# Kernel optimization log

Hardware: AMD Instinct MI355X
Metric: run time of the kernel (lower is better)

## Reference

```python
import jax, jax.numpy as jnp
import numpy as np

C_IN = 256
C_OUT = 256
NUM_HEADS = 4
C_HEAD = C_OUT // NUM_HEADS  # 64
ALPHA = 0.2
NEG_FILL = -9e15


def setup_inputs() -> dict:
    key = jax.random.key(0)
    k1, k2, k3, k4, k5 = jax.random.split(key, 5)
    B, N = 1, 4096
    node_feats = jax.random.normal(k1, (B, N, C_IN), dtype=jnp.float32)
    adj_matrix = jax.random.randint(k2, (B, N, N), 0, 2, dtype=jnp.int32)
    # xavier_uniform with gain=1.414 on projection weight (fan_in=C_IN, fan_out=C_OUT)
    lim_w = 1.414 * np.sqrt(6.0 / (C_IN + C_OUT))
    W = jax.random.uniform(k3, (C_IN, C_OUT), dtype=jnp.float32, minval=-lim_w, maxval=lim_w)
    b = jnp.zeros((C_OUT,), dtype=jnp.float32)
    lim_a = 1.414 * np.sqrt(6.0 / (NUM_HEADS + 2 * C_HEAD))
    a = jax.random.uniform(k4, (NUM_HEADS, 2 * C_HEAD), dtype=jnp.float32, minval=-lim_a, maxval=lim_a)
    return {"node_feats": node_feats, "adj_matrix": adj_matrix, "W": W, "b": b, "a": a}


def reference(node_feats, adj_matrix, W, b, a):
    B, N, _ = node_feats.shape
    # linear projection -> (B, N, H, C_HEAD)
    feats = (node_feats @ W + b).reshape(B, N, NUM_HEADS, C_HEAD)
    # attention logit for edge (i -> j): a_src . h_i + a_dst . h_j, per head
    a_src, a_dst = a[:, :C_HEAD], a[:, C_HEAD:]
    src = jnp.einsum('bnhc,hc->bnh', feats, a_src)  # indexed by row i
    dst = jnp.einsum('bnhc,hc->bnh', feats, a_dst)  # indexed by col j
    logits = src[:, :, None, :] + dst[:, None, :, :]  # (B, N, N, H)
    logits = jnp.where(logits >= 0, logits, ALPHA * logits)  # LeakyReLU(0.2)
    attn = jnp.where(adj_matrix[..., None] == 1, logits, NEG_FILL)
    probs = jax.nn.softmax(attn, axis=2)  # softmax over source nodes j
    out = jnp.einsum('bijh,bjhc->bihc', probs, feats)
    return out.reshape(B, N, NUM_HEADS * C_HEAD)  # concat heads
```

## Files before the change

### kernel.cpp

```cpp
#include <hip/hip_runtime.h>

#define NN 4096
#define C 256
#define NH 4
#define CH 64
#define JSPLIT 8
#define JSLICE (NN / JSPLIT)
#define NJT (JSLICE / 32)

typedef float f32x4 __attribute__((ext_vector_type(4)));
typedef __bf16 b16x8 __attribute__((ext_vector_type(8)));
typedef unsigned short u16x8 __attribute__((ext_vector_type(8)));
typedef unsigned int u32x4 __attribute__((ext_vector_type(4)));
typedef int i32x4 __attribute__((ext_vector_type(4)));
typedef _Float16 f16x2 __attribute__((ext_vector_type(2)));

#if __has_builtin(__builtin_amdgcn_raw_buffer_load_v4f32)
#define FBUF 1
#else
#define FBUF 0
#endif

__device__ inline float fast_exp2(float x) {
#if __has_builtin(__builtin_amdgcn_exp2f)
  return __builtin_amdgcn_exp2f(x);
#else
  return exp2f(x);
#endif
}

__device__ inline unsigned pack2bf(float f0, float f1) {
  unsigned u0 = __float_as_uint(f0) + 0x8000u;
  unsigned u1 = __float_as_uint(f1) + 0x8000u;
  return __builtin_amdgcn_perm(u1, u0, 0x07060302u);
}

__device__ inline unsigned cvtpk(float f0, float f1) {
  unsigned r;
  asm("v_cvt_pk_bf16_f32 %0, %1, %2" : "=v"(r) : "v"(f0), "v"(f1));
  return r;
}

__global__ __launch_bounds__(256) void k_prep(
    const float* __restrict__ X, const float* __restrict__ W,
    unsigned short* __restrict__ Xbf, unsigned short* __restrict__ WT) {
  const int b = blockIdx.x, t = threadIdx.x;
  if (b < 1024) {
    const int idx = b * 256 + t;
    const float4 v = ((const float4*)X)[idx];
    uint2 st;
    st.x = pack2bf(v.x, v.y);
    st.y = pack2bf(v.z, v.w);
    ((uint2*)Xbf)[idx] = st;
  } else {
    const int c = b - 1024;
    const float w = W[(size_t)t * C + c];
    WT[(size_t)c * C + t] = (unsigned short)((__float_as_uint(w) + 0x8000u) >> 16);
  }
}

__global__ __launch_bounds__(256) void k_feats(
    const unsigned short* __restrict__ Xbf, const unsigned short* __restrict__ WT,
    const float* __restrict__ bias, const float* __restrict__ av,
    const int* __restrict__ adj, unsigned char* __restrict__ packed,
    unsigned short* __restrict__ F, float2* __restrict__ srcAB,
    float* __restrict__ Ed) {
  if (blockIdx.x >= 256) {
    const int idx = (blockIdx.x - 256) * 256 + threadIdx.x;
    const int4 a0 = *(const int4*)(adj + (size_t)idx * 8);
    const int4 a1 = *(const int4*)(adj + (size_t)idx * 8 + 4);
    unsigned m = 0;
    m |= (a0.x != 0) ? 1u : 0u;   m |= (a0.y != 0) ? 2u : 0u;
    m |= (a0.z != 0) ? 4u : 0u;   m |= (a0.w != 0) ? 8u : 0u;
    m |= (a1.x != 0) ? 16u : 0u;  m |= (a1.y != 0) ? 32u : 0u;
    m |= (a1.z != 0) ? 64u : 0u;  m |= (a1.w != 0) ? 128u : 0u;
    const int newidx = (idx & ~63) | ((idx & 3) << 4) | ((idx >> 2) & 15);
    packed[newidx] = (unsigned char)m;
    return;
  }
  const int i0 = blockIdx.x * 16;
  const int h = threadIdx.x >> 6;
  const int lane = threadIdx.x & 63;
  const int q = lane >> 4, n = lane & 15;
  const int c0 = h * CH;
  const float LOG2E = 1.4426950408889634f;

  const f32x4 zero = {0.f, 0.f, 0.f, 0.f};
  f32x4 acc[4];
#pragma unroll
  for (int g = 0; g < 4; ++g) acc[g] = zero;

  const unsigned short* ap = Xbf + (size_t)(i0 + n) * C + q * 8;
#pragma unroll
  for (int kt = 0; kt < 8; ++kt) {
    const b16x8 aF = __builtin_bit_cast(b16x8, *(const u16x8*)(ap + kt * 32));
#pragma unroll
    for (int g = 0; g < 4; ++g) {
      const b16x8 bF = __builtin_bit_cast(b16x8,
          *(const u16x8*)(WT + (size_t)(c0 + g * 16 + n) * C + kt * 32 + q * 8));
      acc[g] = __builtin_amdgcn_mfma_f32_16x16x32_bf16(aF, bF, acc[g], 0, 0, 0);
    }
  }

  float fb[4][4], asv[4], adv[4];
#pragma unroll
  for (int g = 0; g < 4; ++g) {
    const float bs = bias[c0 + g * 16 + n];
    asv[g] = av[h * 128 + g * 16 + n];
    adv[g] = av[h * 128 + 64 + g * 16 + n];
#pragma unroll
    for (int r = 0; r < 4; ++r) fb[g][r] = acc[g][r] + bs;
  }
  const int jt = i0 >> 5, half = (i0 >> 4) & 1;
  const int qp = half * 2 + (q >> 1);
#pragma unroll
  for (int g = 0; g < 4; ++g) {
    uint2 st;
    st.x = pack2bf(fb[g][0], fb[g][1]);
    st.y = pack2bf(fb[g][2], fb[g][3]);
    *(uint2*)(F + ((size_t)((jt * NH + h) * 4 + g)) * 512 + (qp * 16 + n) * 8 + 4 * (q & 1)) = st;
  }
#pragma unroll
  for (int r = 0; r < 4; ++r) {
    float p = 0.f, d = 0.f;
#pragma unroll
    for (int g = 0; g < 4; ++g) {
      p = fmaf(fb[g][r], asv[g], p);
      d = fmaf(fb[g][r], adv[g], d);
    }
#pragma unroll
    for (int m = 1; m < 16; m <<= 1) {
      p += __shfl_xor(p, m);
      d += __shfl_xor(d, m);
    }
    if (n == 0) {
      const int row = i0 + q * 4 + r;
      const float dL = d * LOG2E;
      Ed[(size_t)h * NN + row] = fast_exp2(dL);
      Ed[(size_t)NH * NN + (size_t)h * NN + row] = fast_exp2(0.2f * dL);
      const float x = p + 16.0f;
      const float m2 = fmaxf(x, 0.2f * x) * LOG2E;
      srcAB[(size_t)row * NH + h] = make_float2(
          fast_exp2(fmaf(p, LOG2E, -m2)),
          fast_exp2(fmaf(0.2f * p, LOG2E, -m2)));
    }
  }
}

__global__ __launch_bounds__(256, 4) void k_attn(
    const unsigned char* __restrict__ packed,
    const unsigned short* __restrict__ F,
    const float2* __restrict__ srcAB, const float* __restrict__ Ed,
    _Float16* __restrict__ pacc, float* __restrict__ lpart) {
  __shared__ float sEd[NH * 2 * JSLICE];

  const int slice = blockIdx.x;
  const int i0 = blockIdx.y * 16;
  const int tid = threadIdx.x;
  const int h = tid >> 6;
  const int lane = tid & 63;
  const int q = lane >> 4, n = lane & 15;
  const int jbase = slice * JSLICE;

#pragma unroll
  for (int v = 0; v < 4; ++v) {
    const int idx = v * 256 + lane * 4;
    const int pl = idx >> 9, j = idx & 511;
    const float4 vv = *(const float4*)(Ed + (size_t)pl * NH * NN
                                       + (size_t)h * NN + jbase + j);
    *(float4*)(&sEd[h * 1024 + idx]) = vv;
  }

  const int r0 = i0 + n;
  const float2 ab0 = srcAB[(size_t)r0 * NH + h];

  const f32x4 zero = {0.f, 0.f, 0.f, 0.f};
  f32x4 acc[4], lacc = zero;
#pragma unroll
  for (int g = 0; g < 4; ++g) acc[g] = zero;

  u16x8 ou;
#pragma unroll
  for (int jj = 0; jj < 8; ++jj) ou[jj] = 0x3F80;
  const b16x8 ones = __builtin_bit_cast(b16x8, ou);

  const u32x4 m4 = *(const u32x4*)(packed + (size_t)r0 * 512 + (jbase >> 3) + q * 16);

#if FBUF
  i32x4 frsrc;
  frsrc[0] = (int)(unsigned)(size_t)F;
  frsrc[1] = (int)(((size_t)F >> 32) & 0xFFFFu);
  frsrc[2] = (int)0xFFFFFFFFu;
  frsrc[3] = 0x00020000;
  const unsigned fvoff =
      ((unsigned)((jbase >> 5) * 16 + h * 4)) * 1024u + (unsigned)lane * 16u;
#else
  const unsigned short* fp = F + ((size_t)((jbase >> 5) * NH + h) * 4) * 512 + lane * 8;
#endif
  const float* sB = &sEd[h * 1024];

  __syncthreads();

#pragma unroll
  for (int jt = 0; jt < NJT; ++jt) {
    const unsigned Mb = (m4[jt >> 2] >> ((jt & 3) * 8)) & 0xffu;

    const int off = jt * 32 + q * 8;
    const f32x4 eA[2] = { *(const f32x4*)(sB + off), *(const f32x4*)(sB + off + 4) };
    const f32x4 eB[2] = { *(const f32x4*)(sB + 512 + off),
                          *(const f32x4*)(sB + 512 + off + 4) };

    u32x4 pk;
#pragma unroll
    for (int hf = 0; hf < 2; ++hf) {
      const f32x4 xa = eA[hf] * ab0.x;
      const f32x4 xb = eB[hf] * ab0.y;
      float e[4];
#pragma unroll
      for (int t2 = 0; t2 < 4; ++t2) {
        const unsigned bit = 1u << (hf * 4 + t2);
        e[t2] = (Mb & bit) ? fmaxf(xa[t2], xb[t2]) : 0.f;
      }
      pk[hf * 2]     = cvtpk(e[0], e[1]);
      pk[hf * 2 + 1] = cvtpk(e[2], e[3]);
    }
    const b16x8 E = __builtin_bit_cast(b16x8, pk);
#pragma unroll
    for (int g = 0; g < 4; ++g) {
#if FBUF
      const f32x4 bv = __builtin_amdgcn_raw_buffer_load_v4f32(
          frsrc, fvoff + (unsigned)jt * 16384u + (unsigned)g * 1024u, 0, 0);
      const b16x8 bF = __builtin_bit_cast(b16x8, bv);
#else
      const b16x8 bF = __builtin_bit_cast(b16x8,
          *(const u16x8*)(fp + (size_t)(jt * NH * 4 + g) * 512));
#endif
      acc[g] = __builtin_amdgcn_mfma_f32_16x16x32_bf16(E, bF, acc[g], 0, 0, 0);
    }
    lacc = __builtin_amdgcn_mfma_f32_16x16x32_bf16(E, ones, lacc, 0, 0, 0);
  }

#pragma unroll
  for (int g = 0; g < 4; ++g)
#pragma unroll
    for (int r = 0; r < 4; ++r) {
      const int col = h * CH + g * 16 + n;
      pacc[((size_t)slice * NN + i0 + q * 4 + r) * C + col] = (_Float16)acc[g][r];
    }
  if (n == 0) {
#pragma unroll
    for (int r = 0; r < 4; ++r)
      lpart[((size_t)slice * NN + i0 + q * 4 + r) * NH + h] = lacc[r];
  }
}

__global__ __launch_bounds__(256) void k_final(
    const _Float16* __restrict__ pacc, const float* __restrict__ lpart,
    float* __restrict__ out) {
  const int t = threadIdx.x;
  const int row = blockIdx.x * 2 + (t >> 7);
  const int tc = t & 127;
  const int c2 = tc * 2;
  const int h = tc >> 5;
  float l = 0.f, sa0 = 0.f, sa1 = 0.f;
#pragma unroll
  for (int sp = 0; sp < JSPLIT; ++sp) {
    l += lpart[((size_t)sp * NN + row) * NH + h];
    const f16x2 v = *(const f16x2*)(pacc + ((size_t)sp * NN + row) * C + c2);
    sa0 += (float)v[0];
    sa1 += (float)v[1];
  }
  const float rl = 1.0f / l;
  *(float2*)(out + (size_t)row * C + c2) = make_float2(sa0 * rl, sa1 * rl);
}

extern "C" void kernel_launch(void* const* d_in, const int* in_sizes, int n_in,
                              void* d_out, int out_size, void* d_ws, size_t ws_size,
                              hipStream_t stream) {
  const float* nf   = (const float*)d_in[0];
  const int* adj    = (const int*)d_in[1];
  const float* W    = (const float*)d_in[2];
  const float* bias = (const float*)d_in[3];
  const float* av   = (const float*)d_in[4];
  float* out = (float*)d_out;

  char* ws = (char*)d_ws;
  unsigned char* packed  = (unsigned char*)ws;
  unsigned short* Xbf    = (unsigned short*)(ws + (2u << 20));
  unsigned short* WT     = (unsigned short*)(ws + (4u << 20));
  unsigned short* F      = (unsigned short*)(ws + (4u << 20) + (256u << 10));
  float2* srcAB = (float2*)(ws + (6u << 20) + (256u << 10));
  float* Ed     = (float*)(ws + (6u << 20) + (384u << 10));
  float* lpart  = (float*)(ws + (6u << 20) + (512u << 10));
  _Float16* pacc = (_Float16*)(ws + (8u << 20));

  k_prep<<<1280, 256, 0, stream>>>(nf, W, Xbf, WT);
  k_feats<<<8448, 256, 0, stream>>>(Xbf, WT, bias, av, adj, packed, F, srcAB, Ed);
  dim3 g2(JSPLIT, NN / 16);
  k_attn<<<g2, 256, 0, stream>>>(packed, F, srcAB, Ed, pacc, lpart);
  k_final<<<NN / 2, 256, 0, stream>>>(pacc, lpart, out);
}
```

Measured before the change: 137.1 us.

## Process two 16-row tiles per attention block to reuse feature loads

Each k_attn block now handles 32 destination rows instead of 16. Every loaded B-fragment of projected features and every shared-memory Ed read feeds two MFMA chains, and the grid shrinks by half. This halves global feature traffic and the per-block Ed staging per output row, at the cost of more accumulator registers, which may lower occupancy under launch_bounds(256,4), and fewer blocks in the grid.

Measured after the change: 135.4 us. Within noise of the previous version (-1.3%).

```diff
diff --git a/kernel.cpp b/kernel.cpp
--- a/kernel.cpp
+++ b/kernel.cpp
@@ -155,7 +155,7 @@
   __shared__ float sEd[NH * 2 * JSLICE];
 
   const int slice = blockIdx.x;
-  const int i0 = blockIdx.y * 16;
+  const int i0 = blockIdx.y * 32;
   const int tid = threadIdx.x;
   const int h = tid >> 6;
   const int lane = tid & 63;
@@ -171,20 +171,22 @@
     *(float4*)(&sEd[h * 1024 + idx]) = vv;
   }
 
-  const int r0 = i0 + n;
+  const int r0 = i0 + n, r1 = i0 + 16 + n;
   const float2 ab0 = srcAB[(size_t)r0 * NH + h];
+  const float2 ab1 = srcAB[(size_t)r1 * NH + h];
 
   const f32x4 zero = {0.f, 0.f, 0.f, 0.f};
-  f32x4 acc[4], lacc = zero;
-#pragma unroll
-  for (int g = 0; g < 4; ++g) acc[g] = zero;
+  f32x4 acc0[4], acc1[4], lacc0 = zero, lacc1 = zero;
+#pragma unroll
+  for (int g = 0; g < 4; ++g) { acc0[g] = zero; acc1[g] = zero; }
 
   u16x8 ou;
 #pragma unroll
   for (int jj = 0; jj < 8; ++jj) ou[jj] = 0x3F80;
   const b16x8 ones = __builtin_bit_cast(b16x8, ou);
 
-  const u32x4 m4 = *(const u32x4*)(packed + (size_t)r0 * 512 + (jbase >> 3) + q * 16);
+  const u32x4 m40 = *(const u32x4*)(packed + (size_t)r0 * 512 + (jbase >> 3) + q * 16);
+  const u32x4 m41 = *(const u32x4*)(packed + (size_t)r1 * 512 + (jbase >> 3) + q * 16);
 
 #if FBUF
   i32x4 frsrc;
@@ -203,28 +205,35 @@
 
 #pragma unroll
   for (int jt = 0; jt < NJT; ++jt) {
-    const unsigned Mb = (m4[jt >> 2] >> ((jt & 3) * 8)) & 0xffu;
+    const unsigned Mb0 = (m40[jt >> 2] >> ((jt & 3) * 8)) & 0xffu;
+    const unsigned Mb1 = (m41[jt >> 2] >> ((jt & 3) * 8)) & 0xffu;
 
     const int off = jt * 32 + q * 8;
     const f32x4 eA[2] = { *(const f32x4*)(sB + off), *(const f32x4*)(sB + off + 4) };
     const f32x4 eB[2] = { *(const f32x4*)(sB + 512 + off),
                           *(const f32x4*)(sB + 512 + off + 4) };
 
-    u32x4 pk;
+    u32x4 pk0, pk1;
 #pragma unroll
     for (int hf = 0; hf < 2; ++hf) {
-      const f32x4 xa = eA[hf] * ab0.x;
-      const f32x4 xb = eB[hf] * ab0.y;
-      float e[4];
+      const f32x4 xa0 = eA[hf] * ab0.x;
+      const f32x4 xb0 = eB[hf] * ab0.y;
+      const f32x4 xa1 = eA[hf] * ab1.x;
+      const f32x4 xb1 = eB[hf] * ab1.y;
+      float e0[4], e1[4];
 #pragma unroll
       for (int t2 = 0; t2 < 4; ++t2) {
         const unsigned bit = 1u << (hf * 4 + t2);
-        e[t2] = (Mb & bit) ? fmaxf(xa[t2], xb[t2]) : 0.f;
+        e0[t2] = (Mb0 & bit) ? fmaxf(xa0[t2], xb0[t2]) : 0.f;
+        e1[t2] = (Mb1 & bit) ? fmaxf(xa1[t2], xb1[t2]) : 0.f;
       }
-      pk[hf * 2]     = cvtpk(e[0], e[1]);
-      pk[hf * 2 + 1] = cvtpk(e[2], e[3]);
-    }
-    const b16x8 E = __builtin_bit_cast(b16x8, pk);
+      pk0[hf * 2]     = cvtpk(e0[0], e0[1]);
+      pk0[hf * 2 + 1] = cvtpk(e0[2], e0[3]);
+      pk1[hf * 2]     = cvtpk(e1[0], e1[1]);
+      pk1[hf * 2 + 1] = cvtpk(e1[2], e1[3]);
+    }
+    const b16x8 E0 = __builtin_bit_cast(b16x8, pk0);
+    const b16x8 E1 = __builtin_bit_cast(b16x8, pk1);
 #pragma unroll
     for (int g = 0; g < 4; ++g) {
 #if FBUF
@@ -235,9 +244,11 @@
       const b16x8 bF = __builtin_bit_cast(b16x8,
           *(const u16x8*)(fp + (size_t)(jt * NH * 4 + g) * 512));
 #endif
-      acc[g] = __builtin_amdgcn_mfma_f32_16x16x32_bf16(E, bF, acc[g], 0, 0, 0);
-    }
-    lacc = __builtin_amdgcn_mfma_f32_16x16x32_bf16(E, ones, lacc, 0, 0, 0);
+      acc0[g] = __builtin_amdgcn_mfma_f32_16x16x32_bf16(E0, bF, acc0[g], 0, 0, 0);
+      acc1[g] = __builtin_amdgcn_mfma_f32_16x16x32_bf16(E1, bF, acc1[g], 0, 0, 0);
+    }
+    lacc0 = __builtin_amdgcn_mfma_f32_16x16x32_bf16(E0, ones, lacc0, 0, 0, 0);
+    lacc1 = __builtin_amdgcn_mfma_f32_16x16x32_bf16(E1, ones, lacc1, 0, 0, 0);
   }
 
 #pragma unroll
@@ -245,12 +256,15 @@
 #pragma unroll
     for (int r = 0; r < 4; ++r) {
       const int col = h * CH + g * 16 + n;
-      pacc[((size_t)slice * NN + i0 + q * 4 + r) * C + col] = (_Float16)acc[g][r];
+      pacc[((size_t)slice * NN + i0 + q * 4 + r) * C + col] = (_Float16)acc0[g][r];
+      pacc[((size_t)slice * NN + i0 + 16 + q * 4 + r) * C + col] = (_Float16)acc1[g][r];
     }
   if (n == 0) {
 #pragma unroll
-    for (int r = 0; r < 4; ++r)
-      lpart[((size_t)slice * NN + i0 + q * 4 + r) * NH + h] = lacc[r];
+    for (int r = 0; r < 4; ++r) {
+      lpart[((size_t)slice * NN + i0 + q * 4 + r) * NH + h] = lacc0[r];
+      lpart[((size_t)slice * NN + i0 + 16 + q * 4 + r) * NH + h] = lacc1[r];
+    }
   }
 }
 
@@ -296,7 +310,7 @@
 
   k_prep<<<1280, 256, 0, stream>>>(nf, W, Xbf, WT);
   k_feats<<<8448, 256, 0, stream>>>(Xbf, WT, bias, av, adj, packed, F, srcAB, Ed);
-  dim3 g2(JSPLIT, NN / 16);
+  dim3 g2(JSPLIT, NN / 32);
   k_attn<<<g2, 256, 0, stream>>>(packed, F, srcAB, Ed, pacc, lpart);
   k_final<<<NN / 2, 256, 0, stream>>>(pacc, lpart, out);
 }
```

## Process four 16-row groups per attention block to reuse F fragments

Applied to the files above, without the earlier changes.

Each k_attn block now covers 64 destination rows instead of 16, computing four bf16 probability fragments per j-tile and applying each loaded F fragment to all four MFMA accumulator sets. This cuts the F reads and the shared Ed staging per output row by four. In exchange it raises register use (sixteen extra accumulators and extra masks), lowers the launch-bounds occupancy target, and shrinks the grid fourfold.

Measured after the change: 135.4 us (median of 2 runs). About the same (-1.3%).

```diff
diff --git a/kernel.cpp b/kernel.cpp
--- a/kernel.cpp
+++ b/kernel.cpp
@@ -147,7 +147,7 @@
   }
 }
 
-__global__ __launch_bounds__(256, 4) void k_attn(
+__global__ __launch_bounds__(256, 2) void k_attn(
     const unsigned char* __restrict__ packed,
     const unsigned short* __restrict__ F,
     const float2* __restrict__ srcAB, const float* __restrict__ Ed,
@@ -155,7 +155,7 @@
   __shared__ float sEd[NH * 2 * JSLICE];
 
   const int slice = blockIdx.x;
-  const int i0 = blockIdx.y * 16;
+  const int i0 = blockIdx.y * 64;
   const int tid = threadIdx.x;
   const int h = tid >> 6;
   const int lane = tid & 63;
@@ -171,20 +171,24 @@
     *(float4*)(&sEd[h * 1024 + idx]) = vv;
   }
 
-  const int r0 = i0 + n;
-  const float2 ab0 = srcAB[(size_t)r0 * NH + h];
-
   const f32x4 zero = {0.f, 0.f, 0.f, 0.f};
-  f32x4 acc[4], lacc = zero;
-#pragma unroll
-  for (int g = 0; g < 4; ++g) acc[g] = zero;
+  float2 ab[4];
+  u32x4 m4[4];
+  f32x4 acc[4][4], lacc[4];
+#pragma unroll
+  for (int rg = 0; rg < 4; ++rg) {
+    const int rr = i0 + rg * 16 + n;
+    ab[rg] = srcAB[(size_t)rr * NH + h];
+    m4[rg] = *(const u32x4*)(packed + (size_t)rr * 512 + (jbase >> 3) + q * 16);
+    lacc[rg] = zero;
+#pragma unroll
+    for (int g = 0; g < 4; ++g) acc[rg][g] = zero;
+  }
 
   u16x8 ou;
 #pragma unroll
   for (int jj = 0; jj < 8; ++jj) ou[jj] = 0x3F80;
   const b16x8 ones = __builtin_bit_cast(b16x8, ou);
-
-  const u32x4 m4 = *(const u32x4*)(packed + (size_t)r0 * 512 + (jbase >> 3) + q * 16);
 
 #if FBUF
   i32x4 frsrc;
@@ -203,28 +207,32 @@
 
 #pragma unroll
   for (int jt = 0; jt < NJT; ++jt) {
-    const unsigned Mb = (m4[jt >> 2] >> ((jt & 3) * 8)) & 0xffu;
-
     const int off = jt * 32 + q * 8;
     const f32x4 eA[2] = { *(const f32x4*)(sB + off), *(const f32x4*)(sB + off + 4) };
     const f32x4 eB[2] = { *(const f32x4*)(sB + 512 + off),
                           *(const f32x4*)(sB + 512 + off + 4) };
 
-    u32x4 pk;
-#pragma unroll
-    for (int hf = 0; hf < 2; ++hf) {
-      const f32x4 xa = eA[hf] * ab0.x;
-      const f32x4 xb = eB[hf] * ab0.y;
-      float e[4];
-#pragma unroll
-      for (int t2 = 0; t2 < 4; ++t2) {
-        const unsigned bit = 1u << (hf * 4 + t2);
-        e[t2] = (Mb & bit) ? fmaxf(xa[t2], xb[t2]) : 0.f;
+    b16x8 E[4];
+#pragma unroll
+    for (int rg = 0; rg < 4; ++rg) {
+      const unsigned Mb = (m4[rg][jt >> 2] >> ((jt & 3) * 8)) & 0xffu;
+      u32x4 pk;
+#pragma unroll
+      for (int hf = 0; hf < 2; ++hf) {
+        const f32x4 xa = eA[hf] * ab[rg].x;
+        const f32x4 xb = eB[hf] * ab[rg].y;
+        float e[4];
+#pragma unroll
+        for (int t2 = 0; t2 < 4; ++t2) {
+          const unsigned bit = 1u << (hf * 4 + t2);
+          e[t2] = (Mb & bit) ? fmaxf(xa[t2], xb[t2]) : 0.f;
+        }
+        pk[hf * 2]     = cvtpk(e[0], e[1]);
+        pk[hf * 2 + 1] = cvtpk(e[2], e[3]);
       }
-      pk[hf * 2]     = cvtpk(e[0], e[1]);
-      pk[hf * 2 + 1] = cvtpk(e[2], e[3]);
-    }
-    const b16x8 E = __builtin_bit_cast(b16x8, pk);
+      E[rg] = __builtin_bit_cast(b16x8, pk);
+    }
+
 #pragma unroll
     for (int g = 0; g < 4; ++g) {
 #if FBUF
@@ -235,22 +243,30 @@
       const b16x8 bF = __builtin_bit_cast(b16x8,
           *(const u16x8*)(fp + (size_t)(jt * NH * 4 + g) * 512));
 #endif
-      acc[g] = __builtin_amdgcn_mfma_f32_16x16x32_bf16(E, bF, acc[g], 0, 0, 0);
-    }
-    lacc = __builtin_amdgcn_mfma_f32_16x16x32_bf16(E, ones, lacc, 0, 0, 0);
-  }
-
-#pragma unroll
-  for (int g = 0; g < 4; ++g)
-#pragma unroll
-    for (int r = 0; r < 4; ++r) {
-      const int col = h * CH + g * 16 + n;
-      pacc[((size_t)slice * NN + i0 + q * 4 + r) * C + col] = (_Float16)acc[g][r];
-    }
-  if (n == 0) {
-#pragma unroll
-    for (int r = 0; r < 4; ++r)
-      lpart[((size_t)slice * NN + i0 + q * 4 + r) * NH + h] = lacc[r];
+#pragma unroll
+      for (int rg = 0; rg < 4; ++rg)
+        acc[rg][g] = __builtin_amdgcn_mfma_f32_16x16x32_bf16(E[rg], bF, acc[rg][g], 0, 0, 0);
+    }
+#pragma unroll
+    for (int rg = 0; rg < 4; ++rg)
+      lacc[rg] = __builtin_amdgcn_mfma_f32_16x16x32_bf16(E[rg], ones, lacc[rg], 0, 0, 0);
+  }
+
+#pragma unroll
+  for (int rg = 0; rg < 4; ++rg) {
+#pragma unroll
+    for (int g = 0; g < 4; ++g)
+#pragma unroll
+      for (int r = 0; r < 4; ++r) {
+        const int col = h * CH + g * 16 + n;
+        pacc[((size_t)slice * NN + i0 + rg * 16 + q * 4 + r) * C + col] =
+            (_Float16)acc[rg][g][r];
+      }
+    if (n == 0) {
+#pragma unroll
+      for (int r = 0; r < 4; ++r)
+        lpart[((size_t)slice * NN + i0 + rg * 16 + q * 4 + r) * NH + h] = lacc[rg][r];
+    }
   }
 }
 
@@ -296,7 +312,7 @@
 
   k_prep<<<1280, 256, 0, stream>>>(nf, W, Xbf, WT);
   k_feats<<<8448, 256, 0, stream>>>(Xbf, WT, bias, av, adj, packed, F, srcAB, Ed);
-  dim3 g2(JSPLIT, NN / 16);
+  dim3 g2(JSPLIT, NN / 64);
   k_attn<<<g2, 256, 0, stream>>>(packed, F, srcAB, Ed, pacc, lpart);
   k_final<<<NN / 2, 256, 0, stream>>>(pacc, lpart, out);
 }
```
